# Optimization experiments

Measured on AMD Instinct MI355X. Metric: run time of the kernel, lower is better.

Reference implementation:

```python
import jax, jax.numpy as jnp
import numpy as np

B, N, M = 32, 8400, 32
NUM_CLASSES = 80
TOP_K = 10
CLS_W, OBJ_W, REG_W = 1.0, 1.0, 5.0
EPS = 1e-7
IMG = 640.0


def setup_inputs() -> dict:
    key = jax.random.key(0)
    k1, k2, k3, k4, k5, k6, k7 = jax.random.split(key, 7)
    # decoded predictions in pixel scale: [cx, cy, w, h, obj_logit, cls_logits...]
    cxy = jax.random.uniform(k1, (B, N, 2), jnp.float32, 0.0, IMG)
    wh = jax.random.uniform(k2, (B, N, 2), jnp.float32, 10.0, 110.0)
    obj = jax.random.normal(k3, (B, N, 1), jnp.float32)
    cls = jax.random.normal(k4, (B, N, NUM_CLASSES), jnp.float32)
    predictions = jnp.concatenate([cxy, wh, obj, cls], axis=-1)  # (B, N, 85)
    # targets: [cls, cx, cy, w, h]
    gcls = jnp.floor(jax.random.uniform(k5, (B, M, 1), jnp.float32, 0.0, float(NUM_CLASSES)))
    gxy = jax.random.uniform(k6, (B, M, 2), jnp.float32, 50.0, IMG - 50.0)
    gwh = jax.random.uniform(k7, (B, M, 2), jnp.float32, 20.0, 120.0)
    targets = jnp.concatenate([gcls, gxy, gwh], axis=-1)  # (B, M, 5)
    return {"predictions": predictions, "targets": targets}


def cxcywh_to_xyxy(b):
    cx, cy, w, h = b[..., 0], b[..., 1], b[..., 2], b[..., 3]
    return jnp.stack([cx - w / 2, cy - h / 2, cx + w / 2, cy + h / 2], axis=-1)


def bce_with_logits(x, t):
    # numerically stable elementwise BCE with logits
    return jnp.maximum(x, 0.0) - x * t + jnp.log1p(jnp.exp(-jnp.abs(x)))


def pairwise_iou(g, p):
    # g: (M,4) xyxy, p: (N,4) xyxy -> (M,N)
    ix1 = jnp.maximum(g[:, None, 0], p[None, :, 0])
    iy1 = jnp.maximum(g[:, None, 1], p[None, :, 1])
    ix2 = jnp.minimum(g[:, None, 2], p[None, :, 2])
    iy2 = jnp.minimum(g[:, None, 3], p[None, :, 3])
    inter = jnp.clip(ix2 - ix1, 0.0) * jnp.clip(iy2 - iy1, 0.0)
    ga = jnp.clip(g[:, 2] - g[:, 0], 0.0) * jnp.clip(g[:, 3] - g[:, 1], 0.0)
    pa = jnp.clip(p[:, 2] - p[:, 0], 0.0) * jnp.clip(p[:, 3] - p[:, 1], 0.0)
    union = ga[:, None] + pa[None, :] - inter + EPS
    return inter / union


def giou(pred, tgt):
    # elementwise GIoU, pred/tgt (N,4) xyxy -> (N,)
    ix1 = jnp.maximum(pred[:, 0], tgt[:, 0]); iy1 = jnp.maximum(pred[:, 1], tgt[:, 1])
    ix2 = jnp.minimum(pred[:, 2], tgt[:, 2]); iy2 = jnp.minimum(pred[:, 3], tgt[:, 3])
    inter = jnp.clip(ix2 - ix1, 0.0) * jnp.clip(iy2 - iy1, 0.0)
    pa = jnp.clip(pred[:, 2] - pred[:, 0], 0.0) * jnp.clip(pred[:, 3] - pred[:, 1], 0.0)
    ta = jnp.clip(tgt[:, 2] - tgt[:, 0], 0.0) * jnp.clip(tgt[:, 3] - tgt[:, 1], 0.0)
    union = pa + ta - inter + EPS
    iou = inter / union
    ex1 = jnp.minimum(pred[:, 0], tgt[:, 0]); ey1 = jnp.minimum(pred[:, 1], tgt[:, 1])
    ex2 = jnp.maximum(pred[:, 2], tgt[:, 2]); ey2 = jnp.maximum(pred[:, 3], tgt[:, 3])
    enclose = (ex2 - ex1) * (ey2 - ey1) + EPS
    return iou - (enclose - union) / enclose


def _image_loss(pred, tgt):
    # pred: (N, 5+C), tgt: (M, 5)
    pbox = pred[:, :4]
    obj_logit = pred[:, 4]
    cls_logit = pred[:, 5:]
    pxyxy = cxcywh_to_xyxy(pbox)
    gcls = tgt[:, 0].astype(jnp.int32)                  # (M,)
    gxyxy = cxcywh_to_xyxy(tgt[:, 1:5])                 # (M,4)

    iou = pairwise_iou(gxyxy, pxyxy)                    # (M,N)

    # center prior: anchor (prediction) centers inside GT boxes
    cx, cy = pbox[:, 0], pbox[:, 1]
    in_box = ((cx[None, :] > gxyxy[:, 0:1]) & (cx[None, :] < gxyxy[:, 2:3]) &
              (cy[None, :] > gxyxy[:, 1:2]) & (cy[None, :] < gxyxy[:, 3:4]))  # (M,N)

    # classification cost: BCE(sqrt(cls_p*obj_p), onehot), decomposed to avoid (M,N,C)
    score = jnp.sqrt(jax.nn.sigmoid(cls_logit) * jax.nn.sigmoid(obj_logit)[:, None])  # (N,C)
    lp = jnp.log(score + EPS)
    lq = jnp.log(1.0 - score + EPS)
    base = -lq.sum(axis=-1)                             # (N,) = sum_c BCE(p, 0)
    cost_cls = base[None, :] - lp[:, gcls].T + lq[:, gcls].T  # (M,N)

    reg_cost = -jnp.log(iou + 1e-8)
    cost = cost_cls + 3.0 * reg_cost + 1e5 * (~in_box).astype(pred.dtype)
    cost = jax.lax.stop_gradient(cost)

    # dynamic-k: k_m = clip(sum of top-k IoUs, min 1)
    iou_sg = jax.lax.stop_gradient(iou) * in_box.astype(pred.dtype)
    topk_ious, _ = jax.lax.top_k(iou_sg, TOP_K)         # (M, TOP_K)
    dyn_k = jnp.clip(topk_ious.sum(-1).astype(jnp.int32), 1, None)  # (M,)

    # per-GT: keep the dyn_k lowest-cost candidates (rank via double argsort)
    ranks = jnp.argsort(jnp.argsort(cost, axis=1), axis=1)
    assigned = (ranks < dyn_k[:, None]) & in_box        # (M,N)

    # conflict resolution: anchor keeps only its lowest-cost GT
    big = jnp.asarray(1e30, pred.dtype)
    cost_masked = jnp.where(assigned, cost, big)
    matched_gt = jnp.argmin(cost_masked, axis=0)        # (N,)
    fg = assigned.any(axis=0)                            # (N,)
    fgf = fg.astype(pred.dtype)

    # objectness loss over all anchors
    obj_l = bce_with_logits(obj_logit, fgf).sum()
    # classification loss on foreground anchors
    onehot = jax.nn.one_hot(gcls[matched_gt], NUM_CLASSES, dtype=pred.dtype)
    cls_l = (bce_with_logits(cls_logit, onehot) * fgf[:, None]).sum()
    mbox = gxyxy[matched_gt]                            # (N,4)
    reg_l = ((1.0 - giou(pxyxy, mbox)) * fgf).sum()
    return cls_l, obj_l, reg_l, fgf.sum()


def reference(predictions, targets):
    cls_l, obj_l, reg_l, nfg = jax.vmap(_image_loss)(predictions, targets)
    num_fg = jnp.maximum(nfg.sum(), 1.0)
    total = (CLS_W * cls_l.sum() + OBJ_W * obj_l.sum() + REG_W * reg_l.sum()) / num_fg
    return total
```

## Files before the change

kernel.cpp:

```cpp
#include <hip/hip_runtime.h>
#include <math.h>

#define BB 32
#define NN 8400
#define MM 32
#define NC 80
#define PD 85
#define TOPK 10
#define CAPG 768
#define KPL 12
#define FLT_BIG 3.4e38f

__device__ __forceinline__ float bcef_(float x, float t) {
    return fmaxf(x, 0.0f) - x * t + log1pf(expf(-fabsf(x)));
}

__device__ __forceinline__ float frcp_(float x)  { return __builtin_amdgcn_rcpf(x); }
__device__ __forceinline__ float fsqrt_(float x) { return __builtin_amdgcn_sqrtf(x); }
__device__ __forceinline__ float fsig_(float x)  { return frcp_(1.0f + __expf(-x)); }

__device__ __forceinline__ float iou_(float4 pb, float gx1, float gy1,
                                      float gx2, float gy2, float ga) {
    float ix1 = fmaxf(gx1, pb.x), iy1 = fmaxf(gy1, pb.y);
    float ix2 = fminf(gx2, pb.z), iy2 = fminf(gy2, pb.w);
    float inter = fmaxf(ix2 - ix1, 0.0f) * fmaxf(iy2 - iy1, 0.0f);
    float pa = fmaxf(pb.z - pb.x, 0.0f) * fmaxf(pb.w - pb.y, 0.0f);
    float uni = ga + pa - inter + 1e-7f;
    return inter * frcp_(uni);
}
__device__ __forceinline__ float cost_(float cl, float so_n, float base_n, float iou) {
    float s = fsqrt_(fsig_(cl) * so_n);
    float lp = __logf(s + 1e-7f);
    float lq = __logf(1.0f - s + 1e-7f);
    return base_n - lp + lq - 3.0f * __logf(iou + 1e-8f);
}

__global__ void __launch_bounds__(256) kA(const float* __restrict__ pred,
                                          const float* __restrict__ tgt,
                                          float4* __restrict__ pxyxy,
                                          float* __restrict__ base,
                                          float* __restrict__ so,
                                          float* __restrict__ objlogit,
                                          unsigned int* __restrict__ inmask,
                                          unsigned int* __restrict__ mask) {
    const int tid = threadIdx.x;
    const int lane = tid & 63, wid = tid >> 6;
    const int rs = lane >> 5, g = lane & 31;
    const int b = blockIdx.y;
    const int tile = blockIdx.x;

    const float* t = tgt + ((size_t)b * MM + g) * 5;
    const float gx1 = t[1] - t[3] * 0.5f, gy1 = t[2] - t[4] * 0.5f;
    const float gx2 = t[1] + t[3] * 0.5f, gy2 = t[2] + t[4] * 0.5f;

    for (int itr = 0; itr < 2; ++itr) {
        const int pl = wid * 2 + itr;
        const int r0 = tile * 16 + pl * 2;
        const size_t off = ((size_t)b * NN + r0) * PD;

        float x0 = pred[off + lane];
        float x1 = pred[off + 64 + lane];

        float cx0 = __shfl(x0, 0), cy0 = __shfl(x0, 1), w0 = __shfl(x0, 2), h0 = __shfl(x0, 3), ol0 = __shfl(x0, 4);
        float cx1 = __shfl(x1, 21), cy1 = __shfl(x1, 22), w1 = __shfl(x1, 23), h1 = __shfl(x1, 24), ol1 = __shfl(x1, 25);
        float so0 = fsig_(ol0), so1 = fsig_(ol1);

        const float cxs = rs ? cx1 : cx0, cys = rs ? cy1 : cy0;
        const bool inb = (cxs > gx1) && (cxs < gx2) && (cys > gy1) && (cys < gy2);
        const unsigned long long bal = __ballot(inb);
        const bool r0a = (bal & 0xFFFFFFFFull) != 0ull;
        const bool r1a = (bal >> 32) != 0ull;

        const size_t gi = (size_t)b * NN + r0;
        if (lane == 0) {
            pxyxy[gi] = make_float4(cx0 - w0 * 0.5f, cy0 - h0 * 0.5f,
                                    cx0 + w0 * 0.5f, cy0 + h0 * 0.5f);
            objlogit[gi] = ol0; so[gi] = so0;
        } else if (lane == 1) {
            pxyxy[gi + 1] = make_float4(cx1 - w1 * 0.5f, cy1 - h1 * 0.5f,
                                        cx1 + w1 * 0.5f, cy1 + h1 * 0.5f);
            objlogit[gi + 1] = ol1; so[gi + 1] = so1;
        } else if (lane == 2) mask[gi] = 0u;
        else if (lane == 3) mask[gi + 1] = 0u;
        else if (lane == 4) inmask[gi] = (unsigned int)(bal & 0xFFFFFFFFull);
        else if (lane == 5) inmask[gi + 1] = (unsigned int)(bal >> 32);

        if (r0a) {
            float a0 = 0.0f;
            if (lane >= 5)  a0 += __logf(1.0f - fsqrt_(fsig_(x0) * so0) + 1e-7f);
            if (lane < 21)  a0 += __logf(1.0f - fsqrt_(fsig_(x1) * so0) + 1e-7f);
            #pragma unroll
            for (int o = 32; o; o >>= 1) a0 += __shfl_xor(a0, o);
            if (lane == 0) base[gi] = -a0;
        }
        if (r1a) {
            float x2 = (lane < 42) ? pred[off + 128 + lane] : 0.0f;
            float a1 = 0.0f;
            if (lane >= 26) a1 += __logf(1.0f - fsqrt_(fsig_(x1) * so1) + 1e-7f);
            if (lane < 42)  a1 += __logf(1.0f - fsqrt_(fsig_(x2) * so1) + 1e-7f);
            #pragma unroll
            for (int o = 32; o; o >>= 1) a1 += __shfl_xor(a1, o);
            if (lane == 0) base[gi + 1] = -a1;
        }
    }
}

__global__ void __launch_bounds__(256) kC(const float* __restrict__ pred,
                                          const float* __restrict__ tgt,
                                          const float4* __restrict__ pxyxy,
                                          const float* __restrict__ base,
                                          const float* __restrict__ so,
                                          const unsigned int* __restrict__ inmask,
                                          unsigned int* __restrict__ mask) {
    const int x_ = blockIdx.x & 7, k_ = blockIdx.x >> 3;
    const int g = k_ & 31, b = ((k_ >> 5) << 3) | x_;
    const int tid = threadIdx.x;
    const int wid = tid >> 6, lane = tid & 63;

    const float* t = tgt + ((size_t)b * MM + g) * 5;
    const int gcls = (int)t[0];
    const float gx1 = t[1] - t[3] * 0.5f, gy1 = t[2] - t[4] * 0.5f;
    const float gx2 = t[1] + t[3] * 0.5f, gy2 = t[2] + t[4] * 0.5f;
    const float ga = fmaxf(gx2 - gx1, 0.0f) * fmaxf(gy2 - gy1, 0.0f);
    const size_t nb = (size_t)b * NN;
    const unsigned int gbit = 1u << g;

    __shared__ float s_iou[CAPG];
    __shared__ float s_cost[CAPG];
    __shared__ int   s_n[CAPG];
    __shared__ int   s_cnt;
    if (tid == 0) s_cnt = 0;
    __syncthreads();

    for (int n = tid; n < NN; n += 256) {
        if (inmask[nb + n] & gbit) {
            float4 pb = pxyxy[nb + n];
            float iou = iou_(pb, gx1, gy1, gx2, gy2, ga);
            float cl = pred[(nb + (size_t)n) * PD + 5 + gcls];
            float co = cost_(cl, so[nb + n], base[nb + n], iou);
            int idx = atomicAdd(&s_cnt, 1);
            if (idx < CAPG) { s_iou[idx] = iou; s_cost[idx] = co; s_n[idx] = n; }
        }
    }
    __syncthreads();

    if (wid != 0) return;
    const int cnt = min(s_cnt, CAPG);

    float riou[KPL], rcost[KPL]; int rn[KPL];
    #pragma unroll
    for (int k = 0; k < KPL; ++k) {
        int i = lane + 64 * k;
        bool v = i < cnt;
        riou[k]  = v ? s_iou[i]  : -1.0f;
        rcost[k] = v ? s_cost[i] : FLT_BIG;
        rn[k]    = v ? s_n[i]    : 0x7fffffff;
    }

    float ssum = 0.0f;
    {
        const int lim = (cnt < TOPK) ? cnt : TOPK;
        for (int p = 0; p < lim; ++p) {
            float bv = -1.0f; int bidx = 0x7fffffff;
            #pragma unroll
            for (int k = 0; k < KPL; ++k)
                if (riou[k] > bv) { bv = riou[k]; bidx = lane + 64 * k; }
            #pragma unroll
            for (int o = 32; o; o >>= 1) {
                float ov = __shfl_xor(bv, o); int oi = __shfl_xor(bidx, o);
                if (ov > bv || (ov == bv && oi < bidx)) { bv = ov; bidx = oi; }
            }
            ssum += bv;
            if ((bidx & 63) == lane) {
                int kk = bidx >> 6;
                #pragma unroll
                for (int k = 0; k < KPL; ++k) if (k == kk) riou[k] = -1.0f;
            }
        }
    }
    int dynk = (int)ssum;
    if (dynk < 1) dynk = 1;
    if (dynk > TOPK) dynk = TOPK;

    {
        const int lim = (cnt < dynk) ? cnt : dynk;
        for (int p = 0; p < lim; ++p) {
            float bv = FLT_BIG; int bn_ = 0x7fffffff; int bidx = -1;
            #pragma unroll
            for (int k = 0; k < KPL; ++k)
                if (rcost[k] < bv || (rcost[k] == bv && rn[k] < bn_)) {
                    bv = rcost[k]; bn_ = rn[k]; bidx = lane + 64 * k;
                }
            #pragma unroll
            for (int o = 32; o; o >>= 1) {
                float ov = __shfl_xor(bv, o);
                int on = __shfl_xor(bn_, o);
                int oi = __shfl_xor(bidx, o);
                if (ov < bv || (ov == bv && on < bn_)) { bv = ov; bn_ = on; bidx = oi; }
            }
            if ((bidx & 63) == lane) {
                int kk = bidx >> 6;
                #pragma unroll
                for (int k = 0; k < KPL; ++k)
                    if (k == kk) { rcost[k] = FLT_BIG; rn[k] = 0x7fffffff; }
            }
            if (lane == 0) atomicOr(&mask[nb + bn_], gbit);
        }
    }
}

__global__ void __launch_bounds__(256) kD(const float* __restrict__ pred,
                   const float* __restrict__ tgt,
                   const float4* __restrict__ pxyxy,
                   const float* __restrict__ base,
                   const float* __restrict__ so,
                   const float* __restrict__ objlogit,
                   const unsigned int* __restrict__ mask,
                   float* __restrict__ partials) {
    const int tid = threadIdx.x;
    const int i0 = blockIdx.x * 256;
    const int i = i0 + tid;
    const int lane = tid & 63, wid = tid >> 6;
    const int b = i / NN;

    float obj_l, cls_l = 0.0f, reg_l = 0.0f, nfg = 0.0f;
    const unsigned int mk = mask[i];
    obj_l = bcef_(objlogit[i], mk ? 1.0f : 0.0f);

    __shared__ int s_list[256];
    __shared__ int s_gcls[256];
    __shared__ int s_wbase[4];
    __shared__ int s_cnt;

    unsigned long long bal = __ballot(mk != 0);
    int wpos = __popcll(bal & ((1ull << lane) - 1ull));
    if (lane == 0) s_wbase[wid] = __popcll(bal);
    __syncthreads();
    if (tid == 0) {
        int acc = 0;
        for (int w = 0; w < 4; ++w) { int t_ = s_wbase[w]; s_wbase[w] = acc; acc += t_; }
        s_cnt = acc;
    }
    __syncthreads();

    if (mk) {
        int e = s_wbase[wid] + wpos;
        s_list[e] = tid;
        nfg = 1.0f;
        float4 pb = pxyxy[i];
        float base_n = base[i], so_n = so[i];
        float best = 3.0e30f; int bg = 0;
        for (int g = 0; g < MM; ++g) {
            if ((mk >> g) & 1u) {
                const float* tg = tgt + ((size_t)b * MM + g) * 5;
                float ggx1 = tg[1] - tg[3] * 0.5f, ggy1 = tg[2] - tg[4] * 0.5f;
                float ggx2 = tg[1] + tg[3] * 0.5f, ggy2 = tg[2] + tg[4] * 0.5f;
                float gga = fmaxf(ggx2 - ggx1, 0.0f) * fmaxf(ggy2 - ggy1, 0.0f);
                float iou = iou_(pb, ggx1, ggy1, ggx2, ggy2, gga);
                float cl = pred[(size_t)i * PD + 5 + (int)tg[0]];
                float cvv = cost_(cl, so_n, base_n, iou);
                if (cvv < best) { best = cvv; bg = g; }
            }
        }
        const float* tm = tgt + ((size_t)b * MM + bg) * 5;
        s_gcls[e] = (int)tm[0];
        float px1 = pb.x, py1 = pb.y, px2 = pb.z, py2 = pb.w;
        float tx1 = tm[1] - tm[3] * 0.5f, ty1 = tm[2] - tm[4] * 0.5f;
        float tx2 = tm[1] + tm[3] * 0.5f, ty2 = tm[2] + tm[4] * 0.5f;
        float ix1 = fmaxf(px1, tx1), iy1 = fmaxf(py1, ty1);
        float ix2 = fminf(px2, tx2), iy2 = fminf(py2, ty2);
        float inter = fmaxf(ix2 - ix1, 0.0f) * fmaxf(iy2 - iy1, 0.0f);
        float pa = fmaxf(px2 - px1, 0.0f) * fmaxf(py2 - py1, 0.0f);
        float ta = fmaxf(tx2 - tx1, 0.0f) * fmaxf(ty2 - ty1, 0.0f);
        float uni = pa + ta - inter + 1e-7f;
        float iou = inter / uni;
        float ex1 = fminf(px1, tx1), ey1 = fminf(py1, ty1);
        float ex2 = fmaxf(px2, tx2), ey2 = fmaxf(py2, ty2);
        float enclose = (ex2 - ex1) * (ey2 - ey1) + 1e-7f;
        float giou = iou - (enclose - uni) / enclose;
        reg_l = 1.0f - giou;
    }
    __syncthreads();

    const int cnt = s_cnt;
    const int nitems = cnt * NC;
    for (int item = tid; item < nitems; item += 256) {
        int e = item / NC;
        int c = item - e * NC;
        int gi = i0 + s_list[e];
        float x = pred[(size_t)gi * PD + 5 + c];
        cls_l += bcef_(x, (c == s_gcls[e]) ? 1.0f : 0.0f);
    }

    __shared__ float red[256];
    float sums[4] = {cls_l, obj_l, reg_l, nfg};
    float out4[4];
    for (int j = 0; j < 4; ++j) {
        red[tid] = sums[j];
        __syncthreads();
        for (int off = 128; off > 0; off >>= 1) {
            if (tid < off) red[tid] += red[tid + off];
            __syncthreads();
        }
        out4[j] = red[0];
        __syncthreads();
    }
    if (tid == 0) {
        float* pr = partials + (size_t)blockIdx.x * 4;
        pr[0] = out4[0]; pr[1] = out4[1]; pr[2] = out4[2]; pr[3] = out4[3];
    }
}

__global__ void kE(const float* __restrict__ partials, int nblk, float* __restrict__ out) {
    __shared__ float red[256];
    float s[4] = {0, 0, 0, 0};
    for (int i = threadIdx.x; i < nblk; i += 256) {
        s[0] += partials[(size_t)i * 4 + 0];
        s[1] += partials[(size_t)i * 4 + 1];
        s[2] += partials[(size_t)i * 4 + 2];
        s[3] += partials[(size_t)i * 4 + 3];
    }
    float tot[4];
    for (int j = 0; j < 4; ++j) {
        red[threadIdx.x] = s[j];
        __syncthreads();
        for (int off = 128; off > 0; off >>= 1) {
            if (threadIdx.x < off) red[threadIdx.x] += red[threadIdx.x + off];
            __syncthreads();
        }
        tot[j] = red[0];
        __syncthreads();
    }
    if (threadIdx.x == 0) {
        float nfg = fmaxf(tot[3], 1.0f);
        out[0] = (tot[0] + tot[1] + 5.0f * tot[2]) / nfg;
    }
}

extern "C" void kernel_launch(void* const* d_in, const int* in_sizes, int n_in,
                              void* d_out, int out_size, void* d_ws, size_t ws_size,
                              hipStream_t stream) {
    const float* pred = (const float*)d_in[0];
    const float* tgt  = (const float*)d_in[1];
    float* out = (float*)d_out;

    char* ws = (char*)d_ws;
    size_t off = 0;
    float4* pxyxy = (float4*)(ws + off);            off += (size_t)BB * NN * sizeof(float4);
    float* base = (float*)(ws + off);               off += (size_t)BB * NN * sizeof(float);
    float* so = (float*)(ws + off);                 off += (size_t)BB * NN * sizeof(float);
    float* objlogit = (float*)(ws + off);           off += (size_t)BB * NN * sizeof(float);
    unsigned int* inmask = (unsigned int*)(ws + off); off += (size_t)BB * NN * sizeof(unsigned int);
    unsigned int* mask = (unsigned int*)(ws + off); off += (size_t)BB * NN * sizeof(unsigned int);
    float* partials = (float*)(ws + off);

    const int nblk = (BB * NN + 255) / 256;

    dim3 gA(NN / 16, BB);
    kA<<<gA, 256, 0, stream>>>(pred, tgt, pxyxy, base, so, objlogit, inmask, mask);

    kC<<<MM * BB, 256, 0, stream>>>(pred, tgt, pxyxy, base, so, inmask, mask);

    kD<<<nblk, 256, 0, stream>>>(pred, tgt, pxyxy, base, so, objlogit, mask, partials);

    kE<<<1, 256, 0, stream>>>(partials, nblk, out);
}
```

Before: 94.56 us.

## Build per-GT candidate lists in a new kernel instead of rescanning inmask

Adds a kernel kB that, once per image, scans the in-box bitmask and builds a compact list of candidate anchor indices for each GT in shared memory, then writes the lists to the workspace. kC now walks only its GT's compact list instead of scanning all 8400 anchors per (image, GT) block, removing 32x redundant mask reads and the shared atomic counter. The candidate capacity also drops from 768 to 640, which shrinks the per-lane register arrays. The costs are an extra launch and a 32-block kernel with low parallelism and 40KB of shared memory, plus a tighter truncation cap that could change results if an image has more candidates.

```diff
diff --git a/kernel.cpp b/kernel.cpp
--- a/kernel.cpp
+++ b/kernel.cpp
@@ -7,8 +7,8 @@
 #define NC 80
 #define PD 85
 #define TOPK 10
-#define CAPG 768
-#define KPL 12
+#define CAPG 640
+#define KPL 10
 #define FLT_BIG 3.4e38f
 
 __device__ __forceinline__ float bcef_(float x, float t) {
@@ -105,12 +105,43 @@
     }
 }
 
+__global__ void __launch_bounds__(256) kB(const unsigned int* __restrict__ inmask,
+                                          unsigned short* __restrict__ clist,
+                                          int* __restrict__ ccnt) {
+    const int b = blockIdx.x;
+    const int tid = threadIdx.x;
+    __shared__ int lcnt[MM];
+    __shared__ unsigned short llist[MM * CAPG];
+    if (tid < MM) lcnt[tid] = 0;
+    __syncthreads();
+
+    const size_t nb = (size_t)b * NN;
+    for (int n = tid; n < NN; n += 256) {
+        unsigned int m = inmask[nb + n];
+        while (m) {
+            int g = __ffs(m) - 1;
+            m &= m - 1;
+            int idx = atomicAdd(&lcnt[g], 1);
+            if (idx < CAPG) llist[g * CAPG + idx] = (unsigned short)n;
+        }
+    }
+    __syncthreads();
+
+    for (int g = 0; g < MM; ++g) {
+        int c = min(lcnt[g], CAPG);
+        for (int i = tid; i < c; i += 256)
+            clist[((size_t)b * MM + g) * CAPG + i] = llist[g * CAPG + i];
+    }
+    if (tid < MM) ccnt[b * MM + tid] = min(lcnt[tid], CAPG);
+}
+
 __global__ void __launch_bounds__(256) kC(const float* __restrict__ pred,
                                           const float* __restrict__ tgt,
                                           const float4* __restrict__ pxyxy,
                                           const float* __restrict__ base,
                                           const float* __restrict__ so,
-                                          const unsigned int* __restrict__ inmask,
+                                          const unsigned short* __restrict__ clist,
+                                          const int* __restrict__ ccnt,
                                           unsigned int* __restrict__ mask) {
     const int x_ = blockIdx.x & 7, k_ = blockIdx.x >> 3;
     const int g = k_ & 31, b = ((k_ >> 5) << 3) | x_;
@@ -125,27 +156,23 @@
     const size_t nb = (size_t)b * NN;
     const unsigned int gbit = 1u << g;
 
+    const int cnt = min(ccnt[b * MM + g], CAPG);
     __shared__ float s_iou[CAPG];
     __shared__ float s_cost[CAPG];
     __shared__ int   s_n[CAPG];
-    __shared__ int   s_cnt;
-    if (tid == 0) s_cnt = 0;
-    __syncthreads();
-
-    for (int n = tid; n < NN; n += 256) {
-        if (inmask[nb + n] & gbit) {
-            float4 pb = pxyxy[nb + n];
-            float iou = iou_(pb, gx1, gy1, gx2, gy2, ga);
-            float cl = pred[(nb + (size_t)n) * PD + 5 + gcls];
-            float co = cost_(cl, so[nb + n], base[nb + n], iou);
-            int idx = atomicAdd(&s_cnt, 1);
-            if (idx < CAPG) { s_iou[idx] = iou; s_cost[idx] = co; s_n[idx] = n; }
-        }
+
+    const unsigned short* lst = clist + ((size_t)b * MM + g) * CAPG;
+    for (int i = tid; i < cnt; i += 256) {
+        int n = lst[i];
+        float4 pb = pxyxy[nb + n];
+        float iou = iou_(pb, gx1, gy1, gx2, gy2, ga);
+        float cl = pred[(nb + (size_t)n) * PD + 5 + gcls];
+        float co = cost_(cl, so[nb + n], base[nb + n], iou);
+        s_iou[i] = iou; s_cost[i] = co; s_n[i] = n;
     }
     __syncthreads();
 
     if (wid != 0) return;
-    const int cnt = min(s_cnt, CAPG);
 
     float riou[KPL], rcost[KPL]; int rn[KPL];
     #pragma unroll
@@ -352,6 +379,8 @@
     float* objlogit = (float*)(ws + off);           off += (size_t)BB * NN * sizeof(float);
     unsigned int* inmask = (unsigned int*)(ws + off); off += (size_t)BB * NN * sizeof(unsigned int);
     unsigned int* mask = (unsigned int*)(ws + off); off += (size_t)BB * NN * sizeof(unsigned int);
+    unsigned short* clist = (unsigned short*)(ws + off); off += (size_t)BB * MM * CAPG * sizeof(unsigned short);
+    int* ccnt = (int*)(ws + off);                   off += (size_t)BB * MM * sizeof(int);
     float* partials = (float*)(ws + off);
 
     const int nblk = (BB * NN + 255) / 256;
@@ -359,7 +388,9 @@
     dim3 gA(NN / 16, BB);
     kA<<<gA, 256, 0, stream>>>(pred, tgt, pxyxy, base, so, objlogit, inmask, mask);
 
-    kC<<<MM * BB, 256, 0, stream>>>(pred, tgt, pxyxy, base, so, inmask, mask);
+    kB<<<BB, 256, 0, stream>>>(inmask, clist, ccnt);
+
+    kC<<<MM * BB, 256, 0, stream>>>(pred, tgt, pxyxy, base, so, clist, ccnt, mask);
 
     kD<<<nblk, 256, 0, stream>>>(pred, tgt, pxyxy, base, so, objlogit, mask, partials);
 
```

New measurement: 96.84 us. 2.4% more time.
